# Performance work log

Measured on AMD Instinct MI355X. Metric: run time of the kernel, lower is better.

The kernel has to match this reference:

```python
import jax, jax.numpy as jnp
import numpy as np

B, L, F = 8, 1024, 16
N_FEAT = 11  # number of features used for similarity, per nn.Parameter(torch.zeros(11))


def setup_inputs() -> dict:
    key = jax.random.key(0)
    k1, k2, k3 = jax.random.split(key, 3)
    x = jax.random.normal(k1, (B, L, F), dtype=jnp.float32)
    x_lengths = jax.random.randint(k2, (B,), 1, L + 1)  # valid lengths in [1, L]
    # learned parameter; init with small random values so gradients/softmax are non-trivial
    feature_importance = jax.random.normal(k3, (N_FEAT,), dtype=jnp.float32) * 0.1
    return {"x": x, "x_lengths": x_lengths, "feature_importance": feature_importance}


def reference(x, x_lengths, feature_importance):
    # x: (B, L, F); use first 11 features
    xf = x[:, :, :N_FEAT]                                  # (B, L, 11)
    # pairwise weighted L1 feature distance -> (B, L, L)
    diff = jnp.abs(xf[:, :, None, :] - xf[:, None, :, :])  # (B, L, L, 11)
    attn = jnp.einsum('bijk,k->bij', diff, feature_importance)
    # pad masking: mask out key positions j >= length[b]
    seqlen = x.shape[1]
    key_mask = jnp.arange(seqlen)[None, None, :] < x_lengths[:, None, None]  # (B,1,L)
    attn = jnp.where(key_mask, attn, -jnp.inf)
    attn = jax.nn.softmax(attn, axis=-1)
    # masked_fill(isnan, 0) — handles fully-masked rows
    attn = jnp.where(jnp.isnan(attn), jnp.zeros((), attn.dtype), attn)
    return attn
```

## Files before the change

### kernel.cpp

```cpp
#include <hip/hip_runtime.h>
#include <float.h>

#define BATCH 8
#define SEQ   1024
#define FDIM  16
#define NFEAT 11
#define ROWS  16
#define COLS  4

__global__ __launch_bounds__(256, 2)
void featsim_kernel(const float* __restrict__ x,
                    const int* __restrict__ lengths,
                    const float* __restrict__ w,
                    float* __restrict__ out) {
    const int tid = threadIdx.x;
    const int b  = blockIdx.x >> 6;
    const int i0 = (blockIdx.x & 63) * ROWS;
    const int len = lengths[b];

    __shared__ float q_lds[ROWS][12];
    __shared__ float redbuf[4][ROWS];
    __shared__ float rowmax[ROWS];
    __shared__ float rowinv[ROWS];

    if (tid < ROWS * NFEAT) {
        int r = tid / NFEAT, k = tid - r * NFEAT;
        q_lds[r][k] = x[(size_t)(b * SEQ + i0 + r) * FDIM + k];
    }
    __syncthreads();

    float wreg[NFEAT];
    #pragma unroll
    for (int k = 0; k < NFEAT; ++k) wreg[k] = w[k];

    float xj[COLS][12];
    #pragma unroll
    for (int c = 0; c < COLS; ++c) {
        int j = tid + c * 256;
        const float4* p = (const float4*)(x + (size_t)(b * SEQ + j) * FDIM);
        float4 f0 = p[0], f1 = p[1], f2 = p[2];
        xj[c][0] = f0.x; xj[c][1] = f0.y; xj[c][2]  = f0.z; xj[c][3]  = f0.w;
        xj[c][4] = f1.x; xj[c][5] = f1.y; xj[c][6]  = f1.z; xj[c][7]  = f1.w;
        xj[c][8] = f2.x; xj[c][9] = f2.y; xj[c][10] = f2.z; xj[c][11] = f2.w;
    }

    float acc[ROWS][COLS];
    #pragma unroll
    for (int r = 0; r < ROWS; ++r) {
        float qr[NFEAT];
        #pragma unroll
        for (int k = 0; k < NFEAT; ++k) qr[k] = q_lds[r][k];
        #pragma unroll
        for (int c = 0; c < COLS; ++c) {
            float a = 0.f;
            #pragma unroll
            for (int k = 0; k < NFEAT; ++k)
                a += fabsf(qr[k] - xj[c][k]) * wreg[k];
            acc[r][c] = a;
        }
    }

    const int lane = tid & 63;
    const int wv   = tid >> 6;

    #pragma unroll
    for (int r = 0; r < ROWS; ++r) {
        float m = -FLT_MAX;
        #pragma unroll
        for (int c = 0; c < COLS; ++c) {
            int j = tid + c * 256;
            if (j < len) m = fmaxf(m, acc[r][c]);
        }
        #pragma unroll
        for (int o = 32; o > 0; o >>= 1) m = fmaxf(m, __shfl_xor(m, o, 64));
        if (lane == 0) redbuf[wv][r] = m;
    }
    __syncthreads();
    if (tid < ROWS) {
        rowmax[tid] = fmaxf(fmaxf(redbuf[0][tid], redbuf[1][tid]),
                            fmaxf(redbuf[2][tid], redbuf[3][tid]));
    }
    __syncthreads();

    #pragma unroll
    for (int r = 0; r < ROWS; ++r) {
        float m = rowmax[r];
        float s = 0.f;
        #pragma unroll
        for (int c = 0; c < COLS; ++c) {
            int j = tid + c * 256;
            float e = (j < len) ? __expf(acc[r][c] - m) : 0.f;
            acc[r][c] = e;
            s += e;
        }
        #pragma unroll
        for (int o = 32; o > 0; o >>= 1) s += __shfl_xor(s, o, 64);
        if (lane == 0) redbuf[wv][r] = s;
    }
    __syncthreads();
    if (tid < ROWS) {
        float s = redbuf[0][tid] + redbuf[1][tid] + redbuf[2][tid] + redbuf[3][tid];
        rowinv[tid] = 1.f / s;
    }
    __syncthreads();

    #pragma unroll
    for (int r = 0; r < ROWS; ++r) {
        float inv = rowinv[r];
        size_t base = (size_t)(b * SEQ + i0 + r) * SEQ;
        #pragma unroll
        for (int c = 0; c < COLS; ++c)
            out[base + tid + c * 256] = acc[r][c] * inv;
    }
}

extern "C" void kernel_launch(void* const* d_in, const int* in_sizes, int n_in,
                              void* d_out, int out_size, void* d_ws, size_t ws_size,
                              hipStream_t stream) {
    const float* x       = (const float*)d_in[0];
    const int*   lengths = (const int*)d_in[1];
    const float* w       = (const float*)d_in[2];
    float*       out     = (float*)d_out;

    featsim_kernel<<<dim3(BATCH * (SEQ / ROWS)), dim3(256), 0, stream>>>(
        x, lengths, w, out);
}
```

Baseline: 82.50 us.

## Drop softmax max pass, fold log2e into weights, and vectorize output stores

Removes the row-max reduction from the softmax and its two extra barriers. The kernel now exponentiates the weighted distances directly with exp2, using weights pre-scaled by log2(e), and masks invalid keys by multiplying by 0/1. Each thread now owns four contiguous columns, so output rows are written with float4 stores. Rows per block drop to 8 and the occupancy hint rises to 4 blocks. Without max subtraction the exponent can overflow if the weights or feature values are large, so numerical safety depends on the input scale.

```diff
diff --git a/kernel.cpp b/kernel.cpp
--- a/kernel.cpp
+++ b/kernel.cpp
@@ -1,116 +1,114 @@
 #include <hip/hip_runtime.h>
-#include <float.h>
 
 #define BATCH 8
 #define SEQ   1024
 #define FDIM  16
 #define NFEAT 11
-#define ROWS  16
+#define ROWS  8
 #define COLS  4
 
-__global__ __launch_bounds__(256, 2)
+#if __has_builtin(__builtin_amdgcn_exp2f)
+#define EXP2F(x) __builtin_amdgcn_exp2f(x)
+#else
+#define EXP2F(x) exp2f(x)
+#endif
+
+__global__ __launch_bounds__(256, 4)
 void featsim_kernel(const float* __restrict__ x,
                     const int* __restrict__ lengths,
                     const float* __restrict__ w,
                     float* __restrict__ out) {
     const int tid = threadIdx.x;
-    const int b  = blockIdx.x >> 6;
-    const int i0 = (blockIdx.x & 63) * ROWS;
+    const int b   = blockIdx.x >> 7;
+    const int i0  = (blockIdx.x & 127) * ROWS;
     const int len = lengths[b];
 
     __shared__ float q_lds[ROWS][12];
     __shared__ float redbuf[4][ROWS];
-    __shared__ float rowmax[ROWS];
-    __shared__ float rowinv[ROWS];
 
     if (tid < ROWS * NFEAT) {
         int r = tid / NFEAT, k = tid - r * NFEAT;
         q_lds[r][k] = x[(size_t)(b * SEQ + i0 + r) * FDIM + k];
     }
-    __syncthreads();
 
     float wreg[NFEAT];
     #pragma unroll
-    for (int k = 0; k < NFEAT; ++k) wreg[k] = w[k];
-
-    float xj[COLS][12];
-    #pragma unroll
-    for (int c = 0; c < COLS; ++c) {
-        int j = tid + c * 256;
-        const float4* p = (const float4*)(x + (size_t)(b * SEQ + j) * FDIM);
-        float4 f0 = p[0], f1 = p[1], f2 = p[2];
-        xj[c][0] = f0.x; xj[c][1] = f0.y; xj[c][2]  = f0.z; xj[c][3]  = f0.w;
-        xj[c][4] = f1.x; xj[c][5] = f1.y; xj[c][6]  = f1.z; xj[c][7]  = f1.w;
-        xj[c][8] = f2.x; xj[c][9] = f2.y; xj[c][10] = f2.z; xj[c][11] = f2.w;
+    for (int k = 0; k < NFEAT; ++k) {
+        float wv = w[k] * 1.44269504088896340736f;
+        wreg[k] = __uint_as_float(
+            (unsigned)__builtin_amdgcn_readfirstlane(__float_as_uint(wv)));
     }
 
-    float acc[ROWS][COLS];
+    const int j0 = tid * COLS;
+    float xj[COLS][12];
+    {
+        const float4* p = (const float4*)(x + (size_t)(b * SEQ + j0) * FDIM);
+        #pragma unroll
+        for (int c = 0; c < COLS; ++c) {
+            float4 f0 = p[c * 4 + 0], f1 = p[c * 4 + 1], f2 = p[c * 4 + 2];
+            xj[c][0] = f0.x; xj[c][1] = f0.y; xj[c][2]  = f0.z; xj[c][3]  = f0.w;
+            xj[c][4] = f1.x; xj[c][5] = f1.y; xj[c][6]  = f1.z; xj[c][7]  = f1.w;
+            xj[c][8] = f2.x; xj[c][9] = f2.y; xj[c][10] = f2.z;
+        }
+    }
+
+    float vm[COLS];
+    #pragma unroll
+    for (int c = 0; c < COLS; ++c) vm[c] = (j0 + c < len) ? 1.f : 0.f;
+
+    __syncthreads();
+
+    float e[ROWS][COLS];
+    float s[ROWS];
     #pragma unroll
     for (int r = 0; r < ROWS; ++r) {
-        float qr[NFEAT];
-        #pragma unroll
-        for (int k = 0; k < NFEAT; ++k) qr[k] = q_lds[r][k];
+        const float4 q0 = *(const float4*)&q_lds[r][0];
+        const float4 q1 = *(const float4*)&q_lds[r][4];
+        const float4 q2 = *(const float4*)&q_lds[r][8];
+        const float qr[NFEAT] = {q0.x, q0.y, q0.z, q0.w,
+                                 q1.x, q1.y, q1.z, q1.w,
+                                 q2.x, q2.y, q2.z};
         #pragma unroll
         for (int c = 0; c < COLS; ++c) {
             float a = 0.f;
             #pragma unroll
             for (int k = 0; k < NFEAT; ++k)
                 a += fabsf(qr[k] - xj[c][k]) * wreg[k];
-            acc[r][c] = a;
+            e[r][c] = EXP2F(a) * vm[c];
         }
+        s[r] = (e[r][0] + e[r][1]) + (e[r][2] + e[r][3]);
+    }
+
+    #pragma unroll
+    for (int o = 32; o > 0; o >>= 1) {
+        #pragma unroll
+        for (int r = 0; r < ROWS; ++r)
+            s[r] += __shfl_xor(s[r], o, 64);
     }
 
     const int lane = tid & 63;
     const int wv   = tid >> 6;
+    if (lane == 0) {
+        #pragma unroll
+        for (int r = 0; r < ROWS; ++r) redbuf[wv][r] = s[r];
+    }
+    __syncthreads();
+
+    float inv[ROWS];
+    #pragma unroll
+    for (int r = 0; r < ROWS; ++r) {
+        float tot = (redbuf[0][r] + redbuf[1][r]) + (redbuf[2][r] + redbuf[3][r]);
+        inv[r] = __builtin_amdgcn_rcpf(tot);
+    }
 
     #pragma unroll
     for (int r = 0; r < ROWS; ++r) {
-        float m = -FLT_MAX;
-        #pragma unroll
-        for (int c = 0; c < COLS; ++c) {
-            int j = tid + c * 256;
-            if (j < len) m = fmaxf(m, acc[r][c]);
-        }
-        #pragma unroll
-        for (int o = 32; o > 0; o >>= 1) m = fmaxf(m, __shfl_xor(m, o, 64));
-        if (lane == 0) redbuf[wv][r] = m;
-    }
-    __syncthreads();
-    if (tid < ROWS) {
-        rowmax[tid] = fmaxf(fmaxf(redbuf[0][tid], redbuf[1][tid]),
-                            fmaxf(redbuf[2][tid], redbuf[3][tid]));
-    }
-    __syncthreads();
-
-    #pragma unroll
-    for (int r = 0; r < ROWS; ++r) {
-        float m = rowmax[r];
-        float s = 0.f;
-        #pragma unroll
-        for (int c = 0; c < COLS; ++c) {
-            int j = tid + c * 256;
-            float e = (j < len) ? __expf(acc[r][c] - m) : 0.f;
-            acc[r][c] = e;
-            s += e;
-        }
-        #pragma unroll
-        for (int o = 32; o > 0; o >>= 1) s += __shfl_xor(s, o, 64);
-        if (lane == 0) redbuf[wv][r] = s;
-    }
-    __syncthreads();
-    if (tid < ROWS) {
-        float s = redbuf[0][tid] + redbuf[1][tid] + redbuf[2][tid] + redbuf[3][tid];
-        rowinv[tid] = 1.f / s;
-    }
-    __syncthreads();
-
-    #pragma unroll
-    for (int r = 0; r < ROWS; ++r) {
-        float inv = rowinv[r];
-        size_t base = (size_t)(b * SEQ + i0 + r) * SEQ;
-        #pragma unroll
-        for (int c = 0; c < COLS; ++c)
-            out[base + tid + c * 256] = acc[r][c] * inv;
+        float4 o4;
+        o4.x = e[r][0] * inv[r];
+        o4.y = e[r][1] * inv[r];
+        o4.z = e[r][2] * inv[r];
+        o4.w = e[r][3] * inv[r];
+        *(float4*)(out + (size_t)(b * SEQ + i0 + r) * SEQ + j0) = o4;
     }
 }
 
```

Result: faster. 80.61 us (-2.3%).
